# Kernel tuning notes

Measured on AMD Instinct MI355X. Metric: run time of the kernel, lower is better.

Reference implementation:

```python
import jax, jax.numpy as jnp
import numpy as np

D = 4096  # in_features == rotation_size (power of 2 -> K == 1, no extra hadamard_K matmul)


def matmul_hadU(x):
    """Normalized Walsh-Hadamard transform along the last axis, matching the
    torch recursive-butterfly matmul_hadU (K == 1 branch)."""
    n = x.shape[-1]
    shape = x.shape
    v = x.reshape(-1, n, 1)  # (B*, m, c) with m*c == n
    while v.shape[1] > 1:
        b_, m, c = v.shape
        v = v.reshape(b_, m // 2, 2, c)
        a, b = v[:, :, 0, :], v[:, :, 1, :]
        # view(b_, m//2, 2*c): [a+b | a-b] along the channel axis
        v = jnp.concatenate([a + b, a - b], axis=-1)
    return v.reshape(shape) / jnp.sqrt(jnp.asarray(n, x.dtype))


def setup_inputs() -> dict:
    key = jax.random.key(0)
    k_x, k_w, k_b = jax.random.split(key, 3)
    x = jax.random.normal(k_x, (4, 2048, D), dtype=jnp.float32)
    W = jax.random.normal(k_w, (D, D), dtype=jnp.float32) * 0.02  # nn.Linear weight [out, in]
    b = jax.random.normal(k_b, (D,), dtype=jnp.float32) * 0.02
    return {"x": x, "W": W, "b": b}


def reference(x, W, b):
    x_rot = matmul_hadU(x)                 # [B, S, D]
    return jnp.einsum('bsd,od->bso', x_rot, W) + b
```

## Files before the change

### kernel.cpp

```cpp
#include <hip/hip_runtime.h>
#include <hip/hip_bf16.h>


#define D_DIM 4096
#define M_ROWS 8192

typedef float f32x4 __attribute__((ext_vector_type(4)));
typedef __bf16 bf16x8 __attribute__((ext_vector_type(8)));

__device__ __forceinline__ unsigned short f2bf(float f) {
  unsigned int u = __float_as_uint(f);
  return (unsigned short)((u + 0x7fffu + ((u >> 16) & 1u)) >> 16);
}

__device__ __forceinline__ void async16(const void* g, void* l) {
  __builtin_amdgcn_global_load_lds(
      (const __attribute__((address_space(1))) unsigned int*)g,
      (__attribute__((address_space(3))) unsigned int*)l, 16, 0, 0);
}

#define WHT_AS 280
#define WHT_BS 17

__global__ __launch_bounds__(256) void wht_cast_rows(
    const float* __restrict__ X, unsigned short* __restrict__ Y) {
  __shared__ float s[16 * WHT_AS];
  const int row = blockIdx.x;
  const float* xr = X + (size_t)row * D_DIM;
  const int t = threadIdx.x;
  float v[16];

#pragma unroll
  for (int a = 0; a < 16; ++a) v[a] = xr[a * 256 + t];
#pragma unroll
  for (int h = 1; h < 16; h <<= 1) {
#pragma unroll
    for (int i = 0; i < 16; ++i) {
      if ((i & h) == 0) {
        float p = v[i], q = v[i + h];
        v[i] = p + q;
        v[i + h] = p - q;
      }
    }
  }
  {
    const int base = (t >> 4) * WHT_BS + (t & 15);
#pragma unroll
    for (int a = 0; a < 16; ++a) s[a * WHT_AS + base] = v[a];
  }
  __syncthreads();

  {
    const int base = (t >> 4) * WHT_AS + (t & 15);
#pragma unroll
    for (int b = 0; b < 16; ++b) v[b] = s[base + b * WHT_BS];
#pragma unroll
    for (int h = 1; h < 16; h <<= 1) {
#pragma unroll
      for (int i = 0; i < 16; ++i) {
        if ((i & h) == 0) {
          float p = v[i], q = v[i + h];
          v[i] = p + q;
          v[i + h] = p - q;
        }
      }
    }
#pragma unroll
    for (int b = 0; b < 16; ++b) s[base + b * WHT_BS] = v[b];
  }
  __syncthreads();

  {
    const int base = (t >> 4) * WHT_AS + (t & 15) * WHT_BS;
#pragma unroll
    for (int c = 0; c < 16; ++c) v[c] = s[base + c];
#pragma unroll
    for (int h = 1; h < 16; h <<= 1) {
#pragma unroll
      for (int i = 0; i < 16; ++i) {
        if ((i & h) == 0) {
          float p = v[i], q = v[i + h];
          v[i] = p + q;
          v[i + h] = p - q;
        }
      }
    }
    union {
      unsigned short us[16];
      uint4 q4[2];
    } pk;
#pragma unroll
    for (int c = 0; c < 16; ++c) pk.us[c] = f2bf(v[c] * 0.015625f);
    uint4* dst =
        (uint4*)(Y + (size_t)row * D_DIM + (t >> 4) * 256 + (t & 15) * 16);
    dst[0] = pk.q4[0];
    dst[1] = pk.q4[1];
  }
}

__global__ __launch_bounds__(256) void cast_w(const float* __restrict__ W,
                                              unsigned short* __restrict__ Wb) {
  const size_t i = ((size_t)blockIdx.x * 256 + threadIdx.x) * 8;
  const float4* p = (const float4*)(W + i);
  float4 f0 = p[0], f1 = p[1];
  union {
    unsigned short us[8];
    uint4 q;
  } pk;
  pk.us[0] = f2bf(f0.x);
  pk.us[1] = f2bf(f0.y);
  pk.us[2] = f2bf(f0.z);
  pk.us[3] = f2bf(f0.w);
  pk.us[4] = f2bf(f1.x);
  pk.us[5] = f2bf(f1.y);
  pk.us[6] = f2bf(f1.z);
  pk.us[7] = f2bf(f1.w);
  *(uint4*)(Wb + i) = pk.q;
}

__global__ __launch_bounds__(256) void gemm_bt_bias(
    const unsigned short* __restrict__ A,
    const unsigned short* __restrict__ B,
    const float* __restrict__ bias, float* __restrict__ C) {
  constexpr int K = 4096, N = 4096;
  __shared__ unsigned short sA[128 * 32];
  __shared__ unsigned short sB[128 * 32];

  const int tid = threadIdx.x;
  const int lane = tid & 63;
  const int wave = tid >> 6;
  const int wr = wave >> 1;
  const int wc = wave & 1;
  const int row16 = lane & 15;
  const int kgrp = lane >> 4;

  const int m0 = blockIdx.y * 128;
  const int n0 = blockIdx.x * 128;

  const int srow = tid >> 2;
  const int skc = tid & 3;
  const unsigned short* Ag0 = A + (size_t)(m0 + srow) * K + skc * 8;
  const unsigned short* Ag1 = Ag0 + (size_t)64 * K;
  const unsigned short* Bg0 = B + (size_t)(n0 + srow) * K + skc * 8;
  const unsigned short* Bg1 = Bg0 + (size_t)64 * K;
  unsigned short* lA0 = &sA[tid * 8];
  unsigned short* lA1 = &sA[2048 + tid * 8];
  unsigned short* lB0 = &sB[tid * 8];
  unsigned short* lB1 = &sB[2048 + tid * 8];

  f32x4 acc[4][4];
#pragma unroll
  for (int i = 0; i < 4; ++i)
#pragma unroll
    for (int j = 0; j < 4; ++j) acc[i][j] = (f32x4){0.f, 0.f, 0.f, 0.f};

  const int abase = (wr * 64 + row16) * 32 + kgrp * 8;
  const int bbase = (wc * 64 + row16) * 32 + kgrp * 8;

  for (int k0 = 0; k0 < K; k0 += 32) {
    async16(Ag0 + k0, lA0);
    async16(Ag1 + k0, lA1);
    async16(Bg0 + k0, lB0);
    async16(Bg1 + k0, lB1);
    __syncthreads();

    bf16x8 af[4], bfr[4];
#pragma unroll
    for (int mt = 0; mt < 4; ++mt)
      af[mt] = *(const bf16x8*)&sA[abase + mt * 16 * 32];
#pragma unroll
    for (int nt = 0; nt < 4; ++nt)
      bfr[nt] = *(const bf16x8*)&sB[bbase + nt * 16 * 32];
#pragma unroll
    for (int mt = 0; mt < 4; ++mt)
#pragma unroll
      for (int nt = 0; nt < 4; ++nt)
        acc[mt][nt] = __builtin_amdgcn_mfma_f32_16x16x32_bf16(
            af[mt], bfr[nt], acc[mt][nt], 0, 0, 0);
    __syncthreads();
  }

  const int mbase = m0 + wr * 64 + kgrp * 4;
  const int nbase = n0 + wc * 64 + row16;
  float bv[4];
#pragma unroll
  for (int nt = 0; nt < 4; ++nt) bv[nt] = bias[nbase + nt * 16];
#pragma unroll
  for (int mt = 0; mt < 4; ++mt)
#pragma unroll
    for (int nt = 0; nt < 4; ++nt)
#pragma unroll
      for (int r = 0; r < 4; ++r)
        C[(size_t)(mbase + mt * 16 + r) * N + nbase + nt * 16] =
            acc[mt][nt][r] + bv[nt];
}

extern "C" void kernel_launch(void* const* d_in, const int* in_sizes, int n_in,
                              void* d_out, int out_size, void* d_ws,
                              size_t ws_size, hipStream_t stream) {
  const float* x = (const float*)d_in[0];
  const float* W = (const float*)d_in[1];
  const float* b = (const float*)d_in[2];
  float* out = (float*)d_out;

  unsigned short* Xr = (unsigned short*)d_ws;
  unsigned short* Wb = Xr + (size_t)M_ROWS * D_DIM;

  wht_cast_rows<<<M_ROWS, 256, 0, stream>>>(x, Xr);
  cast_w<<<(D_DIM * (size_t)D_DIM / 8) / 256, 256, 0, stream>>>(W, Wb);
  dim3 grid(D_DIM / 128, M_ROWS / 128);
  gemm_bt_bias<<<grid, 256, 0, stream>>>(Xr, Wb, b, out);
}
```

Measured before the change: 559.5 us.

## Replace GEMM with 256x256 double-buffered pipelined kernel with swizzled LDS

```diff
diff --git a/kernel.cpp b/kernel.cpp
--- a/kernel.cpp
+++ b/kernel.cpp
@@ -118,81 +118,155 @@
   *(uint4*)(Wb + i) = pk.q;
 }
 
-__global__ __launch_bounds__(256) void gemm_bt_bias(
+#define GNT 64
+
+__global__ __launch_bounds__(512, 2) void gemm256_bias(
     const unsigned short* __restrict__ A,
     const unsigned short* __restrict__ B,
     const float* __restrict__ bias, float* __restrict__ C) {
   constexpr int K = 4096, N = 4096;
-  __shared__ unsigned short sA[128 * 32];
-  __shared__ unsigned short sB[128 * 32];
+  __shared__ unsigned short sm[65536];
 
   const int tid = threadIdx.x;
-  const int lane = tid & 63;
-  const int wave = tid >> 6;
-  const int wr = wave >> 1;
-  const int wc = wave & 1;
-  const int row16 = lane & 15;
-  const int kgrp = lane >> 4;
-
-  const int m0 = blockIdx.y * 128;
-  const int n0 = blockIdx.x * 128;
-
-  const int srow = tid >> 2;
-  const int skc = tid & 3;
-  const unsigned short* Ag0 = A + (size_t)(m0 + srow) * K + skc * 8;
-  const unsigned short* Ag1 = Ag0 + (size_t)64 * K;
-  const unsigned short* Bg0 = B + (size_t)(n0 + srow) * K + skc * 8;
-  const unsigned short* Bg1 = Bg0 + (size_t)64 * K;
-  unsigned short* lA0 = &sA[tid * 8];
-  unsigned short* lA1 = &sA[2048 + tid * 8];
-  unsigned short* lB0 = &sB[tid * 8];
-  unsigned short* lB1 = &sB[2048 + tid * 8];
-
-  f32x4 acc[4][4];
-#pragma unroll
-  for (int i = 0; i < 4; ++i)
+  const int l = tid & 63;
+  const int w = tid >> 6;
+  const int wm = w >> 2;
+  const int wn = w & 3;
+  const int row16 = l & 15;
+  const int kgrp = l >> 4;
+
+  const int orig = blockIdx.x;
+  const int wgid = (orig & 7) * 64 + (orig >> 3);
+  const int bn = wgid & 15;
+  const int bm = wgid >> 4;
+  const int m0 = bm * 256, n0 = bn * 256;
+
+  const int srcRow = (w >> 1) * 16 + (l >> 2);
+  const int srcCol = (w & 1) * 32 + ((((l & 3) << 4) ^ ((l >> 5) << 5)) >> 1);
+  const unsigned short* aS = A + (size_t)(m0 + srcRow) * K + srcCol;
+  const unsigned short* bS = B + (size_t)(n0 + srcRow) * K + srcCol;
+  const int dstBase = tid * 8;
+
+#define STG_A(b, h, kt)                                                       \
+  do {                                                                        \
+    async16(aS + (size_t)((h)*128) * K + (kt)*64,                             \
+            &sm[(b)*32768 + (h)*8192 + dstBase]);                             \
+    async16(aS + (size_t)((h)*128 + 64) * K + (kt)*64,                        \
+            &sm[(b)*32768 + (h)*8192 + 4096 + dstBase]);                      \
+  } while (0)
+#define STG_B(b, h, kt)                                                       \
+  do {                                                                        \
+    async16(bS + (size_t)((h)*128) * K + (kt)*64,                             \
+            &sm[(b)*32768 + 16384 + (h)*8192 + dstBase]);                     \
+    async16(bS + (size_t)((h)*128 + 64) * K + (kt)*64,                        \
+            &sm[(b)*32768 + 16384 + (h)*8192 + 4096 + dstBase]);              \
+  } while (0)
+
+  const int laneRd = row16 * 32 + ((kgrp << 3) ^ ((row16 >> 3) << 4));
+
+  f32x4 acc[8][4];
+#pragma unroll
+  for (int i = 0; i < 8; ++i)
 #pragma unroll
     for (int j = 0; j < 4; ++j) acc[i][j] = (f32x4){0.f, 0.f, 0.f, 0.f};
 
-  const int abase = (wr * 64 + row16) * 32 + kgrp * 8;
-  const int bbase = (wc * 64 + row16) * 32 + kgrp * 8;
-
-  for (int k0 = 0; k0 < K; k0 += 32) {
-    async16(Ag0 + k0, lA0);
-    async16(Ag1 + k0, lA1);
-    async16(Bg0 + k0, lB0);
-    async16(Bg1 + k0, lB1);
-    __syncthreads();
-
-    bf16x8 af[4], bfr[4];
-#pragma unroll
-    for (int mt = 0; mt < 4; ++mt)
-      af[mt] = *(const bf16x8*)&sA[abase + mt * 16 * 32];
-#pragma unroll
-    for (int nt = 0; nt < 4; ++nt)
-      bfr[nt] = *(const bf16x8*)&sB[bbase + nt * 16 * 32];
-#pragma unroll
-    for (int mt = 0; mt < 4; ++mt)
-#pragma unroll
-      for (int nt = 0; nt < 4; ++nt)
-        acc[mt][nt] = __builtin_amdgcn_mfma_f32_16x16x32_bf16(
-            af[mt], bfr[nt], acc[mt][nt], 0, 0, 0);
-    __syncthreads();
-  }
-
-  const int mbase = m0 + wr * 64 + kgrp * 4;
-  const int nbase = n0 + wc * 64 + row16;
+  STG_A(0, 0, 0);
+  STG_A(0, 1, 0);
+  STG_B(0, 0, 0);
+  STG_B(0, 1, 0);
+  STG_A(1, 0, 1);
+  STG_A(1, 1, 1);
+  STG_B(1, 0, 1);
+  asm volatile("s_waitcnt vmcnt(6)" ::: "memory");
+  __builtin_amdgcn_s_barrier();
+
+#define MFMA1(mf, nf, ks)                                             \
+  acc[mf][nf] = __builtin_amdgcn_mfma_f32_16x16x32_bf16(              \
+      af[mf][ks], bfm[nf][ks], acc[mf][nf], 0, 0, 0)
+#define MFMA_GROUP(g)                                                 \
+  MFMA1(2 * g + 0, 0, 0);                                             \
+  MFMA1(2 * g + 0, 1, 0);                                             \
+  MFMA1(2 * g + 0, 2, 0);                                             \
+  MFMA1(2 * g + 0, 3, 0);                                             \
+  MFMA1(2 * g + 1, 0, 0);                                             \
+  MFMA1(2 * g + 1, 1, 0);                                             \
+  MFMA1(2 * g + 1, 2, 0);                                             \
+  MFMA1(2 * g + 1, 3, 0);                                             \
+  MFMA1(2 * g + 0, 0, 1);                                             \
+  MFMA1(2 * g + 0, 1, 1);                                             \
+  MFMA1(2 * g + 0, 2, 1);                                             \
+  MFMA1(2 * g + 0, 3, 1);                                             \
+  MFMA1(2 * g + 1, 0, 1);                                             \
+  MFMA1(2 * g + 1, 1, 1);                                             \
+  MFMA1(2 * g + 1, 2, 1);                                             \
+  MFMA1(2 * g + 1, 3, 1);
+
+  int cur = 0;
+  for (int T = 0; T < GNT; ++T) {
+    const int base = cur * 32768;
+    const unsigned short* pA = &sm[base + wm * 8192 + laneRd];
+    const unsigned short* pB =
+        &sm[base + 16384 + (wn >> 1) * 8192 + (wn & 1) * 4096 + laneRd];
+
+    bf16x8 af[8][2], bfm[4][2];
+#pragma unroll
+    for (int mf = 0; mf < 8; ++mf) {
+      af[mf][0] = *(const bf16x8*)&pA[mf * 1024];
+      af[mf][1] = *(const bf16x8*)&pA[mf * 1024 + 512];
+    }
+#pragma unroll
+    for (int nf = 0; nf < 4; ++nf) {
+      bfm[nf][0] = *(const bf16x8*)&pB[nf * 1024];
+      bfm[nf][1] = *(const bf16x8*)&pB[nf * 1024 + 512];
+    }
+    if (T + 1 < GNT) STG_B(cur ^ 1, 1, T + 1);
+    __builtin_amdgcn_s_barrier();
+    asm volatile("s_waitcnt lgkmcnt(0)" ::: "memory");
+    __builtin_amdgcn_s_setprio(1);
+    MFMA_GROUP(0);
+    __builtin_amdgcn_s_setprio(0);
+    __builtin_amdgcn_s_barrier();
+
+    if (T + 2 < GNT) STG_A(cur, 0, T + 2);
+    __builtin_amdgcn_s_barrier();
+    __builtin_amdgcn_s_setprio(1);
+    MFMA_GROUP(1);
+    __builtin_amdgcn_s_setprio(0);
+    __builtin_amdgcn_s_barrier();
+
+    if (T + 2 < GNT) STG_A(cur, 1, T + 2);
+    __builtin_amdgcn_s_barrier();
+    __builtin_amdgcn_s_setprio(1);
+    MFMA_GROUP(2);
+    __builtin_amdgcn_s_setprio(0);
+    __builtin_amdgcn_s_barrier();
+
+    if (T + 2 < GNT) STG_B(cur, 0, T + 2);
+    __builtin_amdgcn_s_barrier();
+    __builtin_amdgcn_s_setprio(1);
+    MFMA_GROUP(3);
+    __builtin_amdgcn_s_setprio(0);
+    if (T < GNT - 2)
+      asm volatile("s_waitcnt vmcnt(6)" ::: "memory");
+    else
+      asm volatile("s_waitcnt vmcnt(0)" ::: "memory");
+    __builtin_amdgcn_s_barrier();
+    cur ^= 1;
+  }
+
+  const int mb = m0 + wm * 128 + kgrp * 4;
+  const int nb = n0 + wn * 64 + row16;
   float bv[4];
 #pragma unroll
-  for (int nt = 0; nt < 4; ++nt) bv[nt] = bias[nbase + nt * 16];
-#pragma unroll
-  for (int mt = 0; mt < 4; ++mt)
-#pragma unroll
-    for (int nt = 0; nt < 4; ++nt)
+  for (int nf = 0; nf < 4; ++nf) bv[nf] = bias[nb + nf * 16];
+#pragma unroll
+  for (int mf = 0; mf < 8; ++mf)
+#pragma unroll
+    for (int nf = 0; nf < 4; ++nf)
 #pragma unroll
       for (int r = 0; r < 4; ++r)
-        C[(size_t)(mbase + mt * 16 + r) * N + nbase + nt * 16] =
-            acc[mt][nt][r] + bv[nt];
+        C[(size_t)(mb + mf * 16 + r) * N + nb + nf * 16] =
+            acc[mf][nf][r] + bv[nf];
 }
 
 extern "C" void kernel_launch(void* const* d_in, const int* in_sizes, int n_in,
@@ -208,6 +282,5 @@
 
   wht_cast_rows<<<M_ROWS, 256, 0, stream>>>(x, Xr);
   cast_w<<<(D_DIM * (size_t)D_DIM / 8) / 256, 256, 0, stream>>>(W, Wb);
-  dim3 grid(D_DIM / 128, M_ROWS / 128);
-  gemm_bt_bias<<<grid, 256, 0, stream>>>(Xr, Wb, b, out);
-}
+  gemm256_bias<<<512, 512, 0, stream>>>(Xr, Wb, b, out);
+}
```

After: 496.9 us. -11.2%, faster.

## Replace GEMM with 256x256 double-buffered 32x32x16 MFMA kernel with swizzled LDS

Applied to the files above, without the earlier changes.

```diff
diff --git a/kernel.cpp b/kernel.cpp
--- a/kernel.cpp
+++ b/kernel.cpp
@@ -6,6 +6,7 @@
 #define M_ROWS 8192
 
 typedef float f32x4 __attribute__((ext_vector_type(4)));
+typedef float f32x16 __attribute__((ext_vector_type(16)));
 typedef __bf16 bf16x8 __attribute__((ext_vector_type(8)));
 
 __device__ __forceinline__ unsigned short f2bf(float f) {
@@ -118,81 +119,121 @@
   *(uint4*)(Wb + i) = pk.q;
 }
 
-__global__ __launch_bounds__(256) void gemm_bt_bias(
+#define GNT 64
+
+__global__ __launch_bounds__(256, 1) void gemm256_w4(
     const unsigned short* __restrict__ A,
     const unsigned short* __restrict__ B,
     const float* __restrict__ bias, float* __restrict__ C) {
   constexpr int K = 4096, N = 4096;
-  __shared__ unsigned short sA[128 * 32];
-  __shared__ unsigned short sB[128 * 32];
-
-  const int tid = threadIdx.x;
-  const int lane = tid & 63;
-  const int wave = tid >> 6;
-  const int wr = wave >> 1;
-  const int wc = wave & 1;
-  const int row16 = lane & 15;
-  const int kgrp = lane >> 4;
-
-  const int m0 = blockIdx.y * 128;
-  const int n0 = blockIdx.x * 128;
-
-  const int srow = tid >> 2;
-  const int skc = tid & 3;
-  const unsigned short* Ag0 = A + (size_t)(m0 + srow) * K + skc * 8;
-  const unsigned short* Ag1 = Ag0 + (size_t)64 * K;
-  const unsigned short* Bg0 = B + (size_t)(n0 + srow) * K + skc * 8;
-  const unsigned short* Bg1 = Bg0 + (size_t)64 * K;
-  unsigned short* lA0 = &sA[tid * 8];
-  unsigned short* lA1 = &sA[2048 + tid * 8];
-  unsigned short* lB0 = &sB[tid * 8];
-  unsigned short* lB1 = &sB[2048 + tid * 8];
-
-  f32x4 acc[4][4];
+  __shared__ unsigned short sm[65536];
+
+  const int t = threadIdx.x;
+  const int l = t & 63;
+  const int w = t >> 6;
+  const int wr = w >> 1;
+  const int wc = w & 1;
+  const int r31 = l & 31;
+  const int hi = l >> 5;
+  const int e = l & 7;
+
+  const int orig = blockIdx.x;
+  const int wgid = (orig & 7) * 64 + (orig >> 3);
+  const int bn = wgid & 15;
+  const int bm = wgid >> 4;
+  const int m0 = bm * 256, n0 = bn * 256;
+
+  const int scol = 8 * ((t & 7) ^ ((t >> 3) & 7));
+  const unsigned short* aS = A + (size_t)(m0 + (t >> 3)) * K + scol;
+  const unsigned short* bS = B + (size_t)(n0 + (t >> 3)) * K + scol;
+  const int dstBase = t * 8;
+
+#define STG_T(BUF, KT)                                                    \
+  do {                                                                    \
+    _Pragma("unroll") for (int p = 0; p < 8; ++p)                         \
+        async16(aS + (size_t)(p * 32) * K + (KT)*64,                      \
+                &sm[(BUF)*32768 + p * 2048 + dstBase]);                   \
+    _Pragma("unroll") for (int p = 0; p < 8; ++p)                         \
+        async16(bS + (size_t)(p * 32) * K + (KT)*64,                      \
+                &sm[(BUF)*32768 + 16384 + p * 2048 + dstBase]);           \
+  } while (0)
+
+  int cks[4];
+#pragma unroll
+  for (int k = 0; k < 4; ++k) cks[k] = (((k << 1) | hi) ^ e) * 8;
+  const int aoff = (wr * 128 + r31) * 64;
+  const int boff = 16384 + (wc * 128 + r31) * 64;
+
+  f32x16 acc[4][4];
 #pragma unroll
   for (int i = 0; i < 4; ++i)
 #pragma unroll
-    for (int j = 0; j < 4; ++j) acc[i][j] = (f32x4){0.f, 0.f, 0.f, 0.f};
-
-  const int abase = (wr * 64 + row16) * 32 + kgrp * 8;
-  const int bbase = (wc * 64 + row16) * 32 + kgrp * 8;
-
-  for (int k0 = 0; k0 < K; k0 += 32) {
-    async16(Ag0 + k0, lA0);
-    async16(Ag1 + k0, lA1);
-    async16(Bg0 + k0, lB0);
-    async16(Bg1 + k0, lB1);
-    __syncthreads();
-
-    bf16x8 af[4], bfr[4];
-#pragma unroll
-    for (int mt = 0; mt < 4; ++mt)
-      af[mt] = *(const bf16x8*)&sA[abase + mt * 16 * 32];
-#pragma unroll
-    for (int nt = 0; nt < 4; ++nt)
-      bfr[nt] = *(const bf16x8*)&sB[bbase + nt * 16 * 32];
-#pragma unroll
-    for (int mt = 0; mt < 4; ++mt)
-#pragma unroll
-      for (int nt = 0; nt < 4; ++nt)
-        acc[mt][nt] = __builtin_amdgcn_mfma_f32_16x16x32_bf16(
-            af[mt], bfr[nt], acc[mt][nt], 0, 0, 0);
-    __syncthreads();
-  }
-
-  const int mbase = m0 + wr * 64 + kgrp * 4;
-  const int nbase = n0 + wc * 64 + row16;
+    for (int j = 0; j < 4; ++j)
+#pragma unroll
+      for (int r = 0; r < 16; ++r) acc[i][j][r] = 0.f;
+
+  bf16x8 afr[2][4], bfr[2][4];
+
+#define RD_FRAGS(P, KS, BASE)                                             \
+  do {                                                                    \
+    _Pragma("unroll") for (int mf = 0; mf < 4; ++mf) afr[P][mf] =         \
+        *(const bf16x8*)&sm[(BASE) + aoff + mf * 2048 + cks[KS]];         \
+    _Pragma("unroll") for (int nf = 0; nf < 4; ++nf) bfr[P][nf] =         \
+        *(const bf16x8*)&sm[(BASE) + boff + nf * 2048 + cks[KS]];         \
+  } while (0)
+
+#define MFMA_KS(P)                                                        \
+  do {                                                                    \
+    _Pragma("unroll") for (int mf = 0; mf < 4; ++mf)                      \
+        _Pragma("unroll") for (int nf = 0; nf < 4; ++nf) acc[mf][nf] =    \
+            __builtin_amdgcn_mfma_f32_32x32x16_bf16(                      \
+                afr[P][mf], bfr[P][nf], acc[mf][nf], 0, 0, 0);            \
+  } while (0)
+
+  STG_T(0, 0);
+  STG_T(1, 1);
+  asm volatile("s_waitcnt vmcnt(16)" ::: "memory");
+  __builtin_amdgcn_s_barrier();
+  RD_FRAGS(0, 0, 0);
+
+  int cur = 0;
+  for (int T = 0; T < GNT; ++T) {
+    const int base = cur * 32768;
+
+    RD_FRAGS(1, 1, base);
+    MFMA_KS(0);
+    RD_FRAGS(0, 2, base);
+    MFMA_KS(1);
+    RD_FRAGS(1, 3, base);
+    MFMA_KS(0);
+    MFMA_KS(1);
+
+    asm volatile("s_waitcnt lgkmcnt(0)" ::: "memory");
+    __builtin_amdgcn_s_barrier();
+    if (T + 2 < GNT) STG_T(cur, T + 2);
+    if (T < GNT - 2)
+      asm volatile("s_waitcnt vmcnt(16)" ::: "memory");
+    else
+      asm volatile("s_waitcnt vmcnt(0)" ::: "memory");
+    __builtin_amdgcn_s_barrier();
+    if (T + 1 < GNT) RD_FRAGS(0, 0, base ^ 32768);
+    cur ^= 1;
+  }
+
+  const int mb = m0 + wr * 128;
+  const int ncol = n0 + wc * 128 + r31;
   float bv[4];
 #pragma unroll
-  for (int nt = 0; nt < 4; ++nt) bv[nt] = bias[nbase + nt * 16];
-#pragma unroll
-  for (int mt = 0; mt < 4; ++mt)
-#pragma unroll
-    for (int nt = 0; nt < 4; ++nt)
-#pragma unroll
-      for (int r = 0; r < 4; ++r)
-        C[(size_t)(mbase + mt * 16 + r) * N + nbase + nt * 16] =
-            acc[mt][nt][r] + bv[nt];
+  for (int nf = 0; nf < 4; ++nf) bv[nf] = bias[ncol + nf * 32];
+#pragma unroll
+  for (int mf = 0; mf < 4; ++mf)
+#pragma unroll
+    for (int nf = 0; nf < 4; ++nf)
+#pragma unroll
+      for (int j = 0; j < 16; ++j) {
+        const int row = mb + mf * 32 + (j & 3) + ((j >> 2) << 3) + (hi << 2);
+        C[(size_t)row * N + ncol + nf * 32] = acc[mf][nf][j] + bv[nf];
+      }
 }
 
 extern "C" void kernel_launch(void* const* d_in, const int* in_sizes, int n_in,
@@ -208,6 +249,5 @@
 
   wht_cast_rows<<<M_ROWS, 256, 0, stream>>>(x, Xr);
   cast_w<<<(D_DIM * (size_t)D_DIM / 8) / 256, 256, 0, stream>>>(W, Wb);
-  dim3 grid(D_DIM / 128, M_ROWS / 128);
-  gemm_bt_bias<<<grid, 256, 0, stream>>>(Xr, Wb, b, out);
-}
+  gemm256_w4<<<512, 256, 0, stream>>>(Xr, Wb, b, out);
+}
```

Measured after the change: 543.9 us. 1.03x faster.
